# Kernel tuning notes

Hardware: AMD Instinct MI355X
Metric: run time of the kernel (lower is better)

The kernel has to match this reference:

```python
import jax, jax.numpy as jnp
import numpy as np

N_NODES = 50000
N_EDGES = 600000
VOCAB = 50000
D_IN = 256   # embed.output_size
D = 128      # size


def gcn_conv(x, w, b, src, dst, num_nodes):
    # PyG GCNConv: x' = D^{-1/2} (A + I) D^{-1/2} (x @ W^T) + b
    loop = jnp.arange(num_nodes)
    s = jnp.concatenate([src, loop])
    d = jnp.concatenate([dst, loop])
    x = x @ w.T                                           # [N, D]
    deg = jax.ops.segment_sum(jnp.ones_like(s, x.dtype), d, num_segments=num_nodes)
    dinv = jnp.where(deg > 0, jax.lax.rsqrt(deg), 0.0)
    norm = dinv[s] * dinv[d]                              # [E+N]
    msgs = x[s] * norm[:, None]                           # gather + scale
    out = jax.ops.segment_sum(msgs, d, num_segments=num_nodes)  # scatter-add
    return out + b


def setup_inputs() -> dict:
    key = jax.random.key(0)
    ks = jax.random.split(key, 7)
    node_tokens = jax.random.randint(ks[0], (N_NODES,), 0, VOCAB)
    edge_index = jax.random.randint(ks[1], (2, N_EDGES), 0, N_NODES)
    embed_table = jax.random.normal(ks[2], (VOCAB, D_IN), dtype=jnp.float32) * 0.02
    W_node_w = jax.random.normal(ks[3], (D, D_IN), dtype=jnp.float32) * 0.02
    W_node_b = jnp.zeros((D,), dtype=jnp.float32)
    w1 = jax.random.normal(ks[4], (D, D), dtype=jnp.float32) * 0.02
    b1 = jnp.zeros((D,), dtype=jnp.float32)
    w2 = jax.random.normal(ks[5], (D, D), dtype=jnp.float32) * 0.02
    b2 = jnp.zeros((D,), dtype=jnp.float32)
    return {"node_tokens": node_tokens, "edge_index": edge_index,
            "embed_table": embed_table, "W_node_w": W_node_w, "W_node_b": W_node_b,
            "w1": w1, "b1": b1, "w2": w2, "b2": b2}


def reference(node_tokens, edge_index, embed_table, W_node_w, W_node_b, w1, b1, w2, b2):
    src, dst = edge_index[0], edge_index[1]
    e = embed_table[node_tokens]                 # [N, D_IN] embedding lookup
    x = e @ W_node_w.T + W_node_b                # [N, D]
    x = gcn_conv(x, w1, b1, src, dst, N_NODES)
    x = jax.nn.relu(x)
    x = gcn_conv(x, w2, b2, src, dst, N_NODES)
    return x
```

## Files before the change

kernel.cpp:

```cpp
#include <hip/hip_runtime.h>
#include <hip/hip_bf16.h>

#define N_NODES 50000
#define N_EDGES 600000
#define D_IN 256
#define D 128

#define SCAN_CHUNK 1024
#define N_CHUNKS ((N_NODES + SCAN_CHUNK - 1) / SCAN_CHUNK)
#define GEMM_BLOCKS ((N_NODES + 31) / 32)
#define EDGE_BLOCKS ((N_EDGES + 255) / 256)

typedef unsigned short ushort_t;
typedef __attribute__((ext_vector_type(8))) short bf16x8;
typedef __attribute__((ext_vector_type(16))) float f32x16;

__device__ __forceinline__ float bf2f(ushort_t u) {
  union { unsigned int i; float f; } v;
  v.i = ((unsigned int)u) << 16;
  return v.f;
}
__device__ __forceinline__ ushort_t f2bf(float f) {
  union { float f; unsigned int i; } v;
  v.f = f;
  unsigned int x = v.i;
  unsigned int r = (x + 0x7FFFu + ((x >> 16) & 1u)) >> 16;
  return (ushort_t)r;
}


__global__ __launch_bounds__(256) void k_prep_deg(
    const float* __restrict__ wn, const float* __restrict__ w1,
    const float* __restrict__ bn, const float* __restrict__ w2,
    const float* __restrict__ b1, const float* __restrict__ b2,
    const int* __restrict__ dst,
    ushort_t* __restrict__ WcSw, float* __restrict__ bc,
    ushort_t* __restrict__ W2Sw, float* __restrict__ b1f,
    float* __restrict__ b2f, int* __restrict__ deg) {
  int bid = blockIdx.x;
  if (bid < 128) {
    int j = bid;
    int k = threadIdx.x;
    float acc = 0.f;
    for (int m = 0; m < 128; m++)
      acc += w1[j * 128 + m] * wn[m * 256 + k];
    ushort_t h = f2bf(acc);
    ushort_t l = f2bf(acc - bf2f(h));
    int wv = j >> 5, fm = j & 31;
    int kh = k >> 7, t = (k >> 4) & 7, fq = (k >> 3) & 1, c = k & 7;
    int lane = fq * 32 + fm;
    int base = ((wv * 2 + kh) * 8 + t) * 2 * 512 + lane * 8 + c;
    WcSw[base] = h;
    WcSw[base + 512] = l;
    if (k == 0) {
      float s = 0.f;
      for (int m = 0; m < 128; m++) s += w1[j * 128 + m] * bn[m];
      bc[j] = s;
    }
  } else if (bid < 193) {
    int i = (bid - 128) * 256 + threadIdx.x;
    if (i >= 16640) return;
    if (i < 16384) {
      float v = w2[i];
      ushort_t h = f2bf(v);
      ushort_t l = f2bf(v - bf2f(h));
      int j = i >> 7, k = i & 127;
      int wv = j >> 5, fm = j & 31;
      int t = (k >> 4) & 7, fq = (k >> 3) & 1, c = k & 7;
      int lane = fq * 32 + fm;
      int base = (wv * 8 + t) * 2 * 512 + lane * 8 + c;
      W2Sw[base] = h;
      W2Sw[base + 512] = l;
    } else if (i < 16512) {
      b1f[i - 16384] = b1[i - 16384];
    } else {
      b2f[i - 16512] = b2[i - 16512];
    }
  } else {
    int e = (bid - 193) * 256 + threadIdx.x;
    if (e < N_EDGES) atomicAdd(&deg[dst[e]], 1);
  }
}


__global__ void k_partial(const int* __restrict__ deg, int* __restrict__ partial) {
  __shared__ int lds[256];
  int b = blockIdx.x, t = threadIdx.x;
  int base = b * SCAN_CHUNK + t * 4;
  int s = 0;
#pragma unroll
  for (int i = 0; i < 4; i++) {
    int idx = base + i;
    if (idx < N_NODES) s += deg[idx];
  }
  lds[t] = s;
  __syncthreads();
  for (int off = 128; off > 0; off >>= 1) {
    if (t < off) lds[t] += lds[t + off];
    __syncthreads();
  }
  if (t == 0) partial[b] = lds[0];
}

__global__ void k_scan_final(const int* __restrict__ deg, const int* __restrict__ partial,
                             int* __restrict__ row_start, float* __restrict__ dinv,
                             int* __restrict__ cursor) {
  __shared__ int lds[256];
  __shared__ int plds[64];
  int b = blockIdx.x, t = threadIdx.x;
  if (t < N_CHUNKS) plds[t] = partial[t];
  __syncthreads();
  if (t == 0) {
    int s = 0;
    for (int i = 0; i < b; i++) s += plds[i];
    plds[63] = s;
  }
  int base = b * SCAN_CHUNK + t * 4;
  int v[4];
  int s = 0;
#pragma unroll
  for (int i = 0; i < 4; i++) {
    int idx = base + i;
    v[i] = (idx < N_NODES) ? deg[idx] : 0;
    s += v[i];
  }
  lds[t] = s;
  __syncthreads();
  for (int off = 1; off < 256; off <<= 1) {
    int add = (t >= off) ? lds[t - off] : 0;
    __syncthreads();
    lds[t] += add;
    __syncthreads();
  }
  int excl = lds[t] - s + plds[63];
#pragma unroll
  for (int i = 0; i < 4; i++) {
    int idx = base + i;
    if (idx < N_NODES) {
      row_start[idx] = excl;
      dinv[idx] = rsqrtf((float)(v[i] + 1));
      cursor[idx] = 0;
      excl += v[i];
    }
  }
  if (b == 0 && t == 0) row_start[N_NODES] = N_EDGES;
}

__global__ __launch_bounds__(256) void k_gemm_fill(
    const float* __restrict__ Xv, const int* __restrict__ tokens,
    const ushort_t* __restrict__ Wsw,
    const float* __restrict__ bias, const float* __restrict__ dinvp,
    ushort_t* __restrict__ OutT,
    const int* __restrict__ src, const int* __restrict__ dst,
    const int* __restrict__ row_start, int* __restrict__ cursor,
    int* __restrict__ csr) {
  constexpr int KDIM = D_IN;
  constexpr int KH = KDIM / 128;
  constexpr int XS = KDIM + 8;
  __shared__ __align__(16) ushort_t xh_lds[32 * XS];
  __shared__ __align__(16) ushort_t xl_lds[32 * XS];

  int bid = blockIdx.x;
  if (bid >= GEMM_BLOCKS) {
    int e = (bid - GEMM_BLOCKS) * 256 + threadIdx.x;
    if (e < N_EDGES) {
      int d = dst[e];
      int pos = atomicAdd(&cursor[d], 1);
      csr[row_start[d] + pos] = src[e];
    }
    return;
  }

  int tid = threadIdx.x;
  int lane = tid & 63;
  int wv = tid >> 6;
  int node0 = bid * 32;
  int fm = lane & 31;
  int fq = lane >> 5;

  {
    constexpr int NT = (32 * KDIM / 4) / 256;
    float4 v[NT];
    int rows[NT], cs[NT];
#pragma unroll
    for (int i = 0; i < NT; i++) {
      int seg = tid + 256 * i;
      rows[i] = seg / (KDIM / 4);
      cs[i] = seg % (KDIM / 4);
      int tk = tokens[min(node0 + rows[i], N_NODES - 1)];
      v[i] = *(const float4*)&Xv[(size_t)tk * KDIM + 4 * cs[i]];
    }
#pragma unroll
    for (int i = 0; i < NT; i++) {
      ushort4 h, l;
      h.x = f2bf(v[i].x); l.x = f2bf(v[i].x - bf2f(h.x));
      h.y = f2bf(v[i].y); l.y = f2bf(v[i].y - bf2f(h.y));
      h.z = f2bf(v[i].z); l.z = f2bf(v[i].z - bf2f(h.z));
      h.w = f2bf(v[i].w); l.w = f2bf(v[i].w - bf2f(h.w));
      *(ushort4*)&xh_lds[rows[i] * XS + 4 * cs[i]] = h;
      *(ushort4*)&xl_lds[rows[i] * XS + 4 * cs[i]] = l;
    }
  }
  __syncthreads();

  f32x16 acc;
#pragma unroll
  for (int r = 0; r < 16; r++) acc[r] = 0.f;

#pragma unroll
  for (int kh = 0; kh < KH; kh++) {
    const ushort_t* wb = Wsw + ((size_t)(wv * KH + kh) * 8) * 2 * 512 + lane * 8;
    bf16x8 wbh[8], wbl[8];
#pragma unroll
    for (int t = 0; t < 8; t++) {
      wbh[t] = *(const bf16x8*)(wb + (size_t)t * 1024);
      wbl[t] = *(const bf16x8*)(wb + (size_t)t * 1024 + 512);
    }
#pragma unroll
    for (int t = 0; t < 8; t++) {
      int ko = kh * 128 + t * 16 + fq * 8;
      bf16x8 ah = *(const bf16x8*)&xh_lds[fm * XS + ko];
      bf16x8 al = *(const bf16x8*)&xl_lds[fm * XS + ko];
      acc = __builtin_amdgcn_mfma_f32_32x32x16_bf16(ah, wbh[t], acc, 0, 0, 0);
      acc = __builtin_amdgcn_mfma_f32_32x32x16_bf16(ah, wbl[t], acc, 0, 0, 0);
      acc = __builtin_amdgcn_mfma_f32_32x32x16_bf16(al, wbh[t], acc, 0, 0, 0);
    }
  }
  int j = wv * 32 + fm;
  float bv = bias[j];
#pragma unroll
  for (int r = 0; r < 16; r++) {
    int row = (r & 3) + 8 * (r >> 2) + 4 * fq;
    int node = node0 + row;
    if (node < N_NODES)
      OutT[(size_t)node * D + j] = f2bf((acc[r] + bv) * dinvp[node]);
  }
}

__device__ __forceinline__ void agg_edges(
    const unsigned int* __restrict__ tu, const int* __restrict__ csr,
    int e0, int e1, int lane, float& ax, float& ay) {
  for (int base = e0; base < e1; base += 64) {
    int cnt = min(64, e1 - base);
    int sidx = (lane < cnt) ? csr[base + lane] : 0;
    int i = 0;
    for (; i + 8 <= cnt; i += 8) {
      unsigned int u[8];
#pragma unroll
      for (int q = 0; q < 8; q++) {
        int s = __shfl(sidx, i + q);
        u[q] = tu[(size_t)s * 64 + lane];
      }
#pragma unroll
      for (int q = 0; q < 8; q++) {
        ax += bf2f((ushort_t)(u[q] & 0xFFFF));
        ay += bf2f((ushort_t)(u[q] >> 16));
      }
    }
    for (; i + 4 <= cnt; i += 4) {
      unsigned int u[4];
#pragma unroll
      for (int q = 0; q < 4; q++) {
        int s = __shfl(sidx, i + q);
        u[q] = tu[(size_t)s * 64 + lane];
      }
#pragma unroll
      for (int q = 0; q < 4; q++) {
        ax += bf2f((ushort_t)(u[q] & 0xFFFF));
        ay += bf2f((ushort_t)(u[q] >> 16));
      }
    }
    for (; i < cnt; i++) {
      int s = __shfl(sidx, i);
      unsigned int u = tu[(size_t)s * 64 + lane];
      ax += bf2f((ushort_t)(u & 0xFFFF));
      ay += bf2f((ushort_t)(u >> 16));
    }
  }
}

__global__ __launch_bounds__(256) void k_agg_gemm(
    const ushort_t* __restrict__ t1, const int* __restrict__ row_start,
    const int* __restrict__ csr, const float* __restrict__ dinv,
    const float* __restrict__ b1f,
    const ushort_t* __restrict__ Wsw, ushort_t* __restrict__ OutT2) {
  constexpr int XS = 136;
  __shared__ __align__(16) ushort_t xh_lds[32 * XS];
  __shared__ __align__(16) ushort_t xl_lds[32 * XS];

  int tid = threadIdx.x;
  int lane = tid & 63;
  int wv = tid >> 6;
  int node0 = blockIdx.x * 32;
  int fm = lane & 31;
  int fq = lane >> 5;

  const unsigned int* tu = (const unsigned int*)t1;
  float bx = b1f[2 * lane];
  float by = b1f[2 * lane + 1];

  for (int rr = 0; rr < 8; rr++) {
    int row = wv * 8 + rr;
    int node = node0 + row;
    float ax = 0.f, ay = 0.f;
    if (node < N_NODES) {
      unsigned int u = tu[(size_t)node * 64 + lane];
      ax = bf2f((ushort_t)(u & 0xFFFF));
      ay = bf2f((ushort_t)(u >> 16));
      agg_edges(tu, csr, row_start[node], row_start[node + 1], lane, ax, ay);
      float di = dinv[node];
      ax = fmaxf(di * ax + bx, 0.f);
      ay = fmaxf(di * ay + by, 0.f);
    }
    ushort2 h, l;
    h.x = f2bf(ax); l.x = f2bf(ax - bf2f(h.x));
    h.y = f2bf(ay); l.y = f2bf(ay - bf2f(h.y));
    *(ushort2*)&xh_lds[row * XS + 2 * lane] = h;
    *(ushort2*)&xl_lds[row * XS + 2 * lane] = l;
  }
  __syncthreads();

  f32x16 acc;
#pragma unroll
  for (int r = 0; r < 16; r++) acc[r] = 0.f;
  {
    const ushort_t* wb = Wsw + ((size_t)wv * 8) * 2 * 512 + lane * 8;
    bf16x8 wbh[8], wbl[8];
#pragma unroll
    for (int t = 0; t < 8; t++) {
      wbh[t] = *(const bf16x8*)(wb + (size_t)t * 1024);
      wbl[t] = *(const bf16x8*)(wb + (size_t)t * 1024 + 512);
    }
#pragma unroll
    for (int t = 0; t < 8; t++) {
      int ko = t * 16 + fq * 8;
      bf16x8 ah = *(const bf16x8*)&xh_lds[fm * XS + ko];
      bf16x8 al = *(const bf16x8*)&xl_lds[fm * XS + ko];
      acc = __builtin_amdgcn_mfma_f32_32x32x16_bf16(ah, wbh[t], acc, 0, 0, 0);
      acc = __builtin_amdgcn_mfma_f32_32x32x16_bf16(ah, wbl[t], acc, 0, 0, 0);
      acc = __builtin_amdgcn_mfma_f32_32x32x16_bf16(al, wbh[t], acc, 0, 0, 0);
    }
  }
  int j = wv * 32 + fm;
#pragma unroll
  for (int r = 0; r < 16; r++) {
    int row = (r & 3) + 8 * (r >> 2) + 4 * fq;
    int node = node0 + row;
    if (node < N_NODES)
      OutT2[(size_t)node * D + j] = f2bf(acc[r] * dinv[node]);
  }
}

__global__ __launch_bounds__(256) void k_aggregate_out(
    const ushort_t* __restrict__ t, const int* __restrict__ row_start,
    const int* __restrict__ csr, const float* __restrict__ dinv,
    const float* __restrict__ bias, float* __restrict__ out_f) {
  int wave = threadIdx.x >> 6;
  int lane = threadIdx.x & 63;
  int node = blockIdx.x * 4 + wave;
  if (node >= N_NODES) return;
  const unsigned int* tu = (const unsigned int*)t;
  float ax, ay;
  {
    unsigned int u = tu[(size_t)node * 64 + lane];
    ax = bf2f((ushort_t)(u & 0xFFFF));
    ay = bf2f((ushort_t)(u >> 16));
  }
  agg_edges(tu, csr, row_start[node], row_start[node + 1], lane, ax, ay);
  float di = dinv[node];
  ax = di * ax + bias[2 * lane];
  ay = di * ay + bias[2 * lane + 1];
  float2 o; o.x = ax; o.y = ay;
  *(float2*)&out_f[(size_t)node * D + 2 * lane] = o;
}

extern "C" void kernel_launch(void* const* d_in, const int* in_sizes, int n_in,
                              void* d_out, int out_size, void* d_ws, size_t ws_size,
                              hipStream_t stream) {
  const int* tokens = (const int*)d_in[0];
  const int* edge = (const int*)d_in[1];
  const float* embed = (const float*)d_in[2];
  const float* Wn = (const float*)d_in[3];
  const float* bn = (const float*)d_in[4];
  const float* w1 = (const float*)d_in[5];
  const float* b1 = (const float*)d_in[6];
  const float* w2 = (const float*)d_in[7];
  const float* b2 = (const float*)d_in[8];
  float* out = (float*)d_out;

  const int* src = edge;
  const int* dst = edge + N_EDGES;

  char* ws = (char*)d_ws;
  ushort_t* T1 = (ushort_t*)ws;
  ushort_t* T2 = (ushort_t*)(ws + 12800000);
  float* dinv = (float*)(ws + 38400000);
  int* row_start = (int*)(ws + 38600064);
  int* degcur = (int*)(ws + 38800128);
  int* csr = (int*)(ws + 39200128);
  int* partial = (int*)(ws + 41600192);
  ushort_t* WcSw = (ushort_t*)(ws + 41600512);
  ushort_t* W2Sw = (ushort_t*)(ws + 41731584);
  float* bias_ws = (float*)(ws + 41797120);
  float* bcf = bias_ws;
  float* b1f = bias_ws + 128;
  float* b2f = bias_ws + 256;
  int* deg = degcur;
  int* cursor = degcur + N_NODES;

  hipMemsetAsync(deg, 0, N_NODES * sizeof(int), stream);
  k_prep_deg<<<193 + EDGE_BLOCKS, 256, 0, stream>>>(
      Wn, w1, bn, w2, b1, b2, dst, WcSw, bcf, W2Sw, b1f, b2f, deg);

  k_partial<<<N_CHUNKS, 256, 0, stream>>>(deg, partial);
  k_scan_final<<<N_CHUNKS, 256, 0, stream>>>(deg, partial, row_start, dinv, cursor);

  k_gemm_fill<<<GEMM_BLOCKS + EDGE_BLOCKS, 256, 0, stream>>>(
      embed, tokens, WcSw, bcf, dinv, T1, src, dst, row_start, cursor, csr);

  k_agg_gemm<<<GEMM_BLOCKS, 256, 0, stream>>>(
      T1, row_start, csr, dinv, b1f, W2Sw, T2);

  k_aggregate_out<<<(N_NODES + 3) / 4, 256, 0, stream>>>(
      T2, row_start, csr, dinv, b2f, out);
}
```

Baseline: 245.0 us.

## Gather neighbor rows with 16-byte loads across 4 edge groups; reuse degree atomics for CSR slots

The aggregation now splits each wave into four 16-lane groups. Each group fetches a whole 256-byte bf16 row with uint4 loads, so four edges are processed in parallel per load step, and the partial sums are combined with xor shuffles at the end. Separately, the degree-counting atomic now records each edge's slot within its destination row. This removes the second atomic pass and the cursor reset when building the CSR. The costs are more registers per lane, an extra cross-group reduction, and masked handling of leftover edges.

```diff
diff --git a/kernel.cpp b/kernel.cpp
--- a/kernel.cpp
+++ b/kernel.cpp
@@ -36,7 +36,8 @@
     const int* __restrict__ dst,
     ushort_t* __restrict__ WcSw, float* __restrict__ bc,
     ushort_t* __restrict__ W2Sw, float* __restrict__ b1f,
-    float* __restrict__ b2f, int* __restrict__ deg) {
+    float* __restrict__ b2f, int* __restrict__ deg,
+    int* __restrict__ epos) {
   int bid = blockIdx.x;
   if (bid < 128) {
     int j = bid;
@@ -78,7 +79,7 @@
     }
   } else {
     int e = (bid - 193) * 256 + threadIdx.x;
-    if (e < N_EDGES) atomicAdd(&deg[dst[e]], 1);
+    if (e < N_EDGES) epos[e] = atomicAdd(&deg[dst[e]], 1);
   }
 }
 
@@ -103,8 +104,7 @@
 }
 
 __global__ void k_scan_final(const int* __restrict__ deg, const int* __restrict__ partial,
-                             int* __restrict__ row_start, float* __restrict__ dinv,
-                             int* __restrict__ cursor) {
+                             int* __restrict__ row_start, float* __restrict__ dinv) {
   __shared__ int lds[256];
   __shared__ int plds[64];
   int b = blockIdx.x, t = threadIdx.x;
@@ -139,7 +139,6 @@
     if (idx < N_NODES) {
       row_start[idx] = excl;
       dinv[idx] = rsqrtf((float)(v[i] + 1));
-      cursor[idx] = 0;
       excl += v[i];
     }
   }
@@ -152,7 +151,7 @@
     const float* __restrict__ bias, const float* __restrict__ dinvp,
     ushort_t* __restrict__ OutT,
     const int* __restrict__ src, const int* __restrict__ dst,
-    const int* __restrict__ row_start, int* __restrict__ cursor,
+    const int* __restrict__ row_start, const int* __restrict__ epos,
     int* __restrict__ csr) {
   constexpr int KDIM = D_IN;
   constexpr int KH = KDIM / 128;
@@ -165,8 +164,7 @@
     int e = (bid - GEMM_BLOCKS) * 256 + threadIdx.x;
     if (e < N_EDGES) {
       int d = dst[e];
-      int pos = atomicAdd(&cursor[d], 1);
-      csr[row_start[d] + pos] = src[e];
+      csr[row_start[d] + epos[e]] = src[e];
     }
     return;
   }
@@ -237,44 +235,54 @@
   }
 }
 
-__device__ __forceinline__ void agg_edges(
-    const unsigned int* __restrict__ tu, const int* __restrict__ csr,
-    int e0, int e1, int lane, float& ax, float& ay) {
+__device__ __forceinline__ void addu4(float acc[8], uint4 u) {
+  acc[0] += bf2f((ushort_t)(u.x & 0xFFFFu));
+  acc[1] += bf2f((ushort_t)(u.x >> 16));
+  acc[2] += bf2f((ushort_t)(u.y & 0xFFFFu));
+  acc[3] += bf2f((ushort_t)(u.y >> 16));
+  acc[4] += bf2f((ushort_t)(u.z & 0xFFFFu));
+  acc[5] += bf2f((ushort_t)(u.z >> 16));
+  acc[6] += bf2f((ushort_t)(u.w & 0xFFFFu));
+  acc[7] += bf2f((ushort_t)(u.w >> 16));
+}
+
+__device__ __forceinline__ void agg_edges4(
+    const uint4* __restrict__ tu4, const int* __restrict__ csr,
+    int e0, int e1, int lane, int g, int h, float acc[8]) {
   for (int base = e0; base < e1; base += 64) {
     int cnt = min(64, e1 - base);
     int sidx = (lane < cnt) ? csr[base + lane] : 0;
     int i = 0;
+    for (; i + 32 <= cnt; i += 32) {
+      uint4 u[8];
+#pragma unroll
+      for (int q = 0; q < 8; q++) {
+        int s = __shfl(sidx, i + 4 * q + g);
+        u[q] = tu4[(size_t)s * 16 + h];
+      }
+#pragma unroll
+      for (int q = 0; q < 8; q++) addu4(acc, u[q]);
+    }
     for (; i + 8 <= cnt; i += 8) {
-      unsigned int u[8];
-#pragma unroll
-      for (int q = 0; q < 8; q++) {
-        int s = __shfl(sidx, i + q);
-        u[q] = tu[(size_t)s * 64 + lane];
+      uint4 u[2];
+#pragma unroll
+      for (int q = 0; q < 2; q++) {
+        int s = __shfl(sidx, i + 4 * q + g);
+        u[q] = tu4[(size_t)s * 16 + h];
       }
-#pragma unroll
-      for (int q = 0; q < 8; q++) {
-        ax += bf2f((ushort_t)(u[q] & 0xFFFF));
-        ay += bf2f((ushort_t)(u[q] >> 16));
-      }
+      addu4(acc, u[0]);
+      addu4(acc, u[1]);
     }
     for (; i + 4 <= cnt; i += 4) {
-      unsigned int u[4];
-#pragma unroll
-      for (int q = 0; q < 4; q++) {
-        int s = __shfl(sidx, i + q);
-        u[q] = tu[(size_t)s * 64 + lane];
-      }
-#pragma unroll
-      for (int q = 0; q < 4; q++) {
-        ax += bf2f((ushort_t)(u[q] & 0xFFFF));
-        ay += bf2f((ushort_t)(u[q] >> 16));
-      }
-    }
-    for (; i < cnt; i++) {
-      int s = __shfl(sidx, i);
-      unsigned int u = tu[(size_t)s * 64 + lane];
-      ax += bf2f((ushort_t)(u & 0xFFFF));
-      ay += bf2f((ushort_t)(u >> 16));
+      int s = __shfl(sidx, i + g);
+      uint4 u = tu4[(size_t)s * 16 + h];
+      addu4(acc, u);
+    }
+    if (i < cnt) {
+      int r = cnt - i;
+      int s = __shfl(sidx, (g < r) ? (i + g) : i);
+      uint4 u = tu4[(size_t)s * 16 + h];
+      if (g < r) addu4(acc, u);
     }
   }
 }
@@ -294,29 +302,53 @@
   int node0 = blockIdx.x * 32;
   int fm = lane & 31;
   int fq = lane >> 5;
-
-  const unsigned int* tu = (const unsigned int*)t1;
-  float bx = b1f[2 * lane];
-  float by = b1f[2 * lane + 1];
+  int g = lane >> 4;
+  int h = lane & 15;
+
+  const uint4* tu4 = (const uint4*)t1;
+  float4 bA = *(const float4*)&b1f[h * 8];
+  float4 bB = *(const float4*)&b1f[h * 8 + 4];
 
   for (int rr = 0; rr < 8; rr++) {
     int row = wv * 8 + rr;
     int node = node0 + row;
-    float ax = 0.f, ay = 0.f;
+    float acc[8];
+#pragma unroll
+    for (int q = 0; q < 8; q++) acc[q] = 0.f;
+    if (node < N_NODES)
+      agg_edges4(tu4, csr, row_start[node], row_start[node + 1], lane, g, h, acc);
+#pragma unroll
+    for (int q = 0; q < 8; q++) {
+      acc[q] += __shfl_xor(acc[q], 16);
+      acc[q] += __shfl_xor(acc[q], 32);
+    }
+    float v[8];
     if (node < N_NODES) {
-      unsigned int u = tu[(size_t)node * 64 + lane];
-      ax = bf2f((ushort_t)(u & 0xFFFF));
-      ay = bf2f((ushort_t)(u >> 16));
-      agg_edges(tu, csr, row_start[node], row_start[node + 1], lane, ax, ay);
+      addu4(acc, tu4[(size_t)node * 16 + h]);
       float di = dinv[node];
-      ax = fmaxf(di * ax + bx, 0.f);
-      ay = fmaxf(di * ay + by, 0.f);
-    }
-    ushort2 h, l;
-    h.x = f2bf(ax); l.x = f2bf(ax - bf2f(h.x));
-    h.y = f2bf(ay); l.y = f2bf(ay - bf2f(h.y));
-    *(ushort2*)&xh_lds[row * XS + 2 * lane] = h;
-    *(ushort2*)&xl_lds[row * XS + 2 * lane] = l;
+      v[0] = fmaxf(di * acc[0] + bA.x, 0.f);
+      v[1] = fmaxf(di * acc[1] + bA.y, 0.f);
+      v[2] = fmaxf(di * acc[2] + bA.z, 0.f);
+      v[3] = fmaxf(di * acc[3] + bA.w, 0.f);
+      v[4] = fmaxf(di * acc[4] + bB.x, 0.f);
+      v[5] = fmaxf(di * acc[5] + bB.y, 0.f);
+      v[6] = fmaxf(di * acc[6] + bB.z, 0.f);
+      v[7] = fmaxf(di * acc[7] + bB.w, 0.f);
+    } else {
+#pragma unroll
+      for (int q = 0; q < 8; q++) v[q] = 0.f;
+    }
+    if (g < 2) {
+      bf16x8 pack;
+#pragma unroll
+      for (int q = 0; q < 8; q++) {
+        ushort_t hq = f2bf(v[q]);
+        pack[q] = (short)((g == 0) ? hq : f2bf(v[q] - bf2f(hq)));
+      }
+      ushort_t* dstp = (g == 0) ? &xh_lds[row * XS + h * 8]
+                                : &xl_lds[row * XS + h * 8];
+      *(bf16x8*)dstp = pack;
+    }
   }
   __syncthreads();
 
@@ -359,19 +391,37 @@
   int lane = threadIdx.x & 63;
   int node = blockIdx.x * 4 + wave;
   if (node >= N_NODES) return;
-  const unsigned int* tu = (const unsigned int*)t;
-  float ax, ay;
-  {
-    unsigned int u = tu[(size_t)node * 64 + lane];
-    ax = bf2f((ushort_t)(u & 0xFFFF));
-    ay = bf2f((ushort_t)(u >> 16));
-  }
-  agg_edges(tu, csr, row_start[node], row_start[node + 1], lane, ax, ay);
+  int g = lane >> 4;
+  int h = lane & 15;
+  const uint4* tu4 = (const uint4*)t;
+  float acc[8];
+#pragma unroll
+  for (int q = 0; q < 8; q++) acc[q] = 0.f;
+  agg_edges4(tu4, csr, row_start[node], row_start[node + 1], lane, g, h, acc);
+#pragma unroll
+  for (int q = 0; q < 8; q++) {
+    acc[q] += __shfl_xor(acc[q], 16);
+    acc[q] += __shfl_xor(acc[q], 32);
+  }
+  addu4(acc, tu4[(size_t)node * 16 + h]);
   float di = dinv[node];
-  ax = di * ax + bias[2 * lane];
-  ay = di * ay + bias[2 * lane + 1];
-  float2 o; o.x = ax; o.y = ay;
-  *(float2*)&out_f[(size_t)node * D + 2 * lane] = o;
+  float4 bA = *(const float4*)&bias[h * 8];
+  float4 bB = *(const float4*)&bias[h * 8 + 4];
+  if (g == 0) {
+    float4 o;
+    o.x = di * acc[0] + bA.x;
+    o.y = di * acc[1] + bA.y;
+    o.z = di * acc[2] + bA.z;
+    o.w = di * acc[3] + bA.w;
+    *(float4*)&out_f[(size_t)node * D + h * 8] = o;
+  } else if (g == 1) {
+    float4 o;
+    o.x = di * acc[4] + bB.x;
+    o.y = di * acc[5] + bB.y;
+    o.z = di * acc[6] + bB.z;
+    o.w = di * acc[7] + bB.w;
+    *(float4*)&out_f[(size_t)node * D + h * 8 + 4] = o;
+  }
 }
 
 extern "C" void kernel_launch(void* const* d_in, const int* in_sizes, int n_in,
@@ -394,9 +444,10 @@
   char* ws = (char*)d_ws;
   ushort_t* T1 = (ushort_t*)ws;
   ushort_t* T2 = (ushort_t*)(ws + 12800000);
+  int* epos = (int*)(ws + 25600000);
   float* dinv = (float*)(ws + 38400000);
   int* row_start = (int*)(ws + 38600064);
-  int* degcur = (int*)(ws + 38800128);
+  int* deg = (int*)(ws + 38800128);
   int* csr = (int*)(ws + 39200128);
   int* partial = (int*)(ws + 41600192);
   ushort_t* WcSw = (ushort_t*)(ws + 41600512);
@@ -405,18 +456,16 @@
   float* bcf = bias_ws;
   float* b1f = bias_ws + 128;
   float* b2f = bias_ws + 256;
-  int* deg = degcur;
-  int* cursor = degcur + N_NODES;
 
   hipMemsetAsync(deg, 0, N_NODES * sizeof(int), stream);
   k_prep_deg<<<193 + EDGE_BLOCKS, 256, 0, stream>>>(
-      Wn, w1, bn, w2, b1, b2, dst, WcSw, bcf, W2Sw, b1f, b2f, deg);
+      Wn, w1, bn, w2, b1, b2, dst, WcSw, bcf, W2Sw, b1f, b2f, deg, epos);
 
   k_partial<<<N_CHUNKS, 256, 0, stream>>>(deg, partial);
-  k_scan_final<<<N_CHUNKS, 256, 0, stream>>>(deg, partial, row_start, dinv, cursor);
+  k_scan_final<<<N_CHUNKS, 256, 0, stream>>>(deg, partial, row_start, dinv);
 
   k_gemm_fill<<<GEMM_BLOCKS + EDGE_BLOCKS, 256, 0, stream>>>(
-      embed, tokens, WcSw, bcf, dinv, T1, src, dst, row_start, cursor, csr);
+      embed, tokens, WcSw, bcf, dinv, T1, src, dst, row_start, epos, csr);
 
   k_agg_gemm<<<GEMM_BLOCKS, 256, 0, stream>>>(
       T1, row_start, csr, dinv, b1f, W2Sw, T2);
```

Result: slower. 258.5 us (+5.5%).
